# Kernel optimization log

Hardware: AMD Instinct MI355X
Metric: run time of the kernel (lower is better)

The kernel has to match this reference:

```python
import jax, jax.numpy as jnp
from jax import lax
import numpy as np

DIM = 256
QK = 256          # qk_dim defaults to dim
HEADS = 8
NWIN = 7
TOPK = 4
KS = 3            # side_dwconv


def setup_inputs() -> dict:
    key = jax.random.key(0)
    ks = jax.random.split(key, 8)
    B, H, W = 1, 112, 112
    s = lambda d: 1.0 / np.sqrt(d)
    return {
        "x": jax.random.normal(ks[0], (B, H, W, DIM), jnp.float32),
        # fused qkv linear: dim -> qk + qk + dim
        "w_qkv": jax.random.normal(ks[1], (DIM, 2 * QK + DIM), jnp.float32) * s(DIM),
        "b_qkv": jnp.zeros((2 * QK + DIM,), jnp.float32),
        # output projection
        "w_o": jax.random.normal(ks[2], (DIM, DIM), jnp.float32) * s(DIM),
        "b_o": jnp.zeros((DIM,), jnp.float32),
        # depthwise 3x3 lepe conv (HWIO with I=1, groups=dim)
        "lepe_w": jax.random.normal(ks[3], (KS, KS, 1, DIM), jnp.float32) * s(KS * KS),
        "lepe_b": jnp.zeros((DIM,), jnp.float32),
    }


def _win2img(t, B, H, W, c):
    # (B, p2, h, w, c) windows -> (B, H, W, c) image
    hw, ww = H // NWIN, W // NWIN
    t = t.reshape(B, NWIN, NWIN, hw, ww, c)
    return t.transpose(0, 1, 3, 2, 4, 5).reshape(B, H, W, c)


def reference(x, w_qkv, b_qkv, w_o, b_o, lepe_w, lepe_b):
    B, H, W, C = x.shape
    hw, ww = H // NWIN, W // NWIN
    p2, w2 = NWIN * NWIN, hw * ww
    hd_q, hd_v = QK // HEADS, DIM // HEADS
    scale = QK ** (-0.5)

    # partition into windows: (B, p2, hw, ww, C)
    xp = x.reshape(B, NWIN, hw, NWIN, ww, C).transpose(0, 1, 3, 2, 4, 5)
    xp = xp.reshape(B, p2, hw, ww, C)

    qkv = xp @ w_qkv + b_qkv
    q, kv = qkv[..., :QK], qkv[..., QK:]          # (B,p2,hw,ww,QK), (...,QK+DIM)

    q_pix = q.reshape(B, p2, w2, QK)
    kv_pix = kv.reshape(B, p2, w2, QK + DIM)      # identity kv_down

    # region-level routing (detached in original since diff_routing=False)
    q_win = lax.stop_gradient(q.mean((2, 3)))     # (B,p2,QK)
    k_win = lax.stop_gradient(kv[..., :QK].mean((2, 3)))
    logit = (q_win * scale) @ jnp.swapaxes(k_win, -1, -2)   # (B,p2,p2)
    top_logit, top_idx = lax.top_k(logit, TOPK)             # (B,p2,TOPK)
    r_weight = jax.nn.softmax(top_logit, axis=-1)           # unused: mul_weight='none'

    # gather top-k regions' KV: (B, p2, TOPK, w2, QK+DIM)
    kv_sel = jax.vmap(lambda kvb, idxb: kvb[idxb])(kv_pix, top_idx)

    k_sel = kv_sel[..., :QK].reshape(B, p2, TOPK * w2, HEADS, hd_q)
    v_sel = kv_sel[..., QK:].reshape(B, p2, TOPK * w2, HEADS, hd_v)
    qh = q_pix.reshape(B, p2, w2, HEADS, hd_q)

    attn = jnp.einsum('bpqhc,bpkhc->bphqk', qh * scale, k_sel)
    attn = jax.nn.softmax(attn, axis=-1)
    out = jnp.einsum('bphqk,bpkhc->bpqhc', attn, v_sel).reshape(B, p2, hw, ww, DIM)
    out = _win2img(out, B, H, W, DIM)

    # lepe: depthwise conv over v in image layout
    v_img = _win2img(kv[..., QK:], B, H, W, DIM)
    lepe = lax.conv_general_dilated(
        v_img, lepe_w, (1, 1), 'SAME',
        dimension_numbers=('NHWC', 'HWIO', 'NHWC'),
        feature_group_count=DIM) + lepe_b

    return (out + lepe) @ w_o + b_o
```

## Files before the change

### kernel.cpp

```cpp
#include <hip/hip_runtime.h>
#include <math.h>


typedef __bf16 bf16x8 __attribute__((ext_vector_type(8)));
typedef __bf16 bf16x4 __attribute__((ext_vector_type(4)));
typedef float f32x4 __attribute__((ext_vector_type(4)));

__global__ __launch_bounds__(64)
void pack1(const float* __restrict__ w_qkv, const float* __restrict__ w_o,
           __bf16* __restrict__ wtq, __bf16* __restrict__ wto,
           float* __restrict__ qkwin) {
    const int b = blockIdx.x;
    const int t = threadIdx.x;
    if (b < 768) {
        int n = b;
        int k = t * 4;
        bf16x4 o;
        o[0] = (__bf16)w_qkv[(k + 0) * 768 + n];
        o[1] = (__bf16)w_qkv[(k + 1) * 768 + n];
        o[2] = (__bf16)w_qkv[(k + 2) * 768 + n];
        o[3] = (__bf16)w_qkv[(k + 3) * 768 + n];
        *(bf16x4*)(wtq + (size_t)n * 256 + k) = o;
    } else if (b < 1024) {
        int n = b - 768;
        int k = t * 4;
        bf16x4 o;
        o[0] = (__bf16)w_o[(k + 0) * 256 + n];
        o[1] = (__bf16)w_o[(k + 1) * 256 + n];
        o[2] = (__bf16)w_o[(k + 2) * 256 + n];
        o[3] = (__bf16)w_o[(k + 3) * 256 + n];
        *(bf16x4*)(wto + (size_t)n * 256 + k) = o;
    } else {
        int idx = (b - 1024) * 64 + t;
        *(float4*)(qkwin + (size_t)idx * 4) = (float4){0.f, 0.f, 0.f, 0.f};
    }
}

template<int QKV>
__global__ __launch_bounds__(256)
void gemm_bf16(const __bf16* __restrict__ A,
               const float* __restrict__ Ax,
               const __bf16* __restrict__ Wt,
               const float* __restrict__ bias,
               float* __restrict__ C, int N,
               __bf16* __restrict__ Qp,
               __bf16* __restrict__ Kp,
               __bf16* __restrict__ vbf,
               __bf16* __restrict__ Vt,
               float* __restrict__ q_win,
               float* __restrict__ k_win) {
    const int t = threadIdx.x & 63;
    const int wv = threadIdx.x >> 6;
    const int l16 = t & 15, quad = t >> 4;
    const int m0 = blockIdx.x * 64;
    const int n0 = blockIdx.y * 128 + wv * 32;

    __shared__ __align__(16) char smem[33792];
    __bf16 (*const As)[264] = (__bf16(*)[264])smem;
    __bf16 (*const Vs)[72]  = (__bf16(*)[72])smem;

    if (QKV == 1) {
        const int p = m0 >> 8, pixbase = m0 & 255;
        const int rowbase0 = (p / 7) * 16 * 112 + (p % 7) * 16;
#pragma unroll
        for (int it = 0; it < 16; it++) {
            const int j = it * 1024 + threadIdx.x * 4;
            const int r = j >> 8, col = j & 255;
            const int pix = pixbase + r;
            const int ir = rowbase0 + (pix >> 4) * 112 + (pix & 15);
            const float4 f = *(const float4*)(Ax + (size_t)ir * 256 + col);
            bf16x4 o;
            o[0] = (__bf16)f.x; o[1] = (__bf16)f.y;
            o[2] = (__bf16)f.z; o[3] = (__bf16)f.w;
            *(bf16x4*)&As[r][col] = o;
        }
    } else {
#pragma unroll
        for (int it = 0; it < 8; it++) {
            const int j = it * 2048 + threadIdx.x * 8;
            const int r = j >> 8, col = j & 255;
            *(bf16x8*)&As[r][col] = *(const bf16x8*)(A + (size_t)(m0 + r) * 256 + col);
        }
    }
    __syncthreads();

    f32x4 acc[2][4];
#pragma unroll
    for (int km = 0; km < 2; km++)
#pragma unroll
        for (int nt = 0; nt < 4; nt++) acc[km][nt] = (f32x4){0.f, 0.f, 0.f, 0.f};

    bf16x8 Afc[2];
#pragma unroll
    for (int km = 0; km < 2; km++)
        Afc[km] = *(const bf16x8*)(Wt + (size_t)(n0 + km * 16 + l16) * 256 + quad * 8);

#pragma unroll
    for (int ks = 0; ks < 8; ks++) {
        bf16x8 Afn[2];
        const int ksn = (ks < 7) ? ks + 1 : 7;
#pragma unroll
        for (int km = 0; km < 2; km++)
            Afn[km] = *(const bf16x8*)(Wt + (size_t)(n0 + km * 16 + l16) * 256 + ksn * 32 + quad * 8);

        bf16x8 Bf[4];
#pragma unroll
        for (int nt = 0; nt < 4; nt++)
            Bf[nt] = *(const bf16x8*)&As[nt * 16 + l16][ks * 32 + quad * 8];

#pragma unroll
        for (int km = 0; km < 2; km++)
#pragma unroll
            for (int nt = 0; nt < 4; nt++)
                acc[km][nt] = __builtin_amdgcn_mfma_f32_16x16x32_bf16(
                    Afc[km], Bf[nt], acc[km][nt], 0, 0, 0);

#pragma unroll
        for (int km = 0; km < 2; km++) Afc[km] = Afn[km];
    }

    if (QKV == 1 && blockIdx.y >= 4) __syncthreads();

    float ws[2][4];
#pragma unroll
    for (int km = 0; km < 2; km++)
#pragma unroll
        for (int j = 0; j < 4; j++) ws[km][j] = 0.f;

#pragma unroll
    for (int km = 0; km < 2; km++) {
        const int n = n0 + km * 16 + quad * 4;
        float4 b4 = *(const float4*)(bias + n);
#pragma unroll
        for (int nt = 0; nt < 4; nt++) {
            const int m = m0 + nt * 16 + l16;
            float v0 = acc[km][nt][0] + b4.x;
            float v1 = acc[km][nt][1] + b4.y;
            float v2 = acc[km][nt][2] + b4.z;
            float v3 = acc[km][nt][3] + b4.w;
            if (QKV == 0) {
                float4 o = {v0, v1, v2, v3};
                *(float4*)(C + (size_t)m * N + n) = o;
            } else {
                const int p = m >> 8, pix = m & 255;
                if (n0 < 512) {
                    ws[km][0] += v0; ws[km][1] += v1;
                    ws[km][2] += v2; ws[km][3] += v3;
                }
                if (n0 < 256) {
                    const float s = 1.4426950408889634f / 16.0f;
                    int h = n >> 5, cc = n & 31;
                    bf16x4 o;
                    o[0] = (__bf16)(v0 * s); o[1] = (__bf16)(v1 * s);
                    o[2] = (__bf16)(v2 * s); o[3] = (__bf16)(v3 * s);
                    *(bf16x4*)(Qp + ((size_t)((p * 8 + h) * 256 + pix)) * 32 + cc) = o;
                } else if (n0 < 512) {
                    int n2 = n - 256;
                    int h = n2 >> 5, cc = n2 & 31;
                    bf16x4 o;
                    o[0] = (__bf16)v0; o[1] = (__bf16)v1;
                    o[2] = (__bf16)v2; o[3] = (__bf16)v3;
                    *(bf16x4*)(Kp + ((size_t)((p * 8 + h) * 256 + pix)) * 32 + cc) = o;
                } else {
                    int n2 = n - 512;
                    int imgrow = ((p / 7) * 16 + (pix >> 4)) * 112 + (p % 7) * 16 + (pix & 15);
                    bf16x4 o;
                    o[0] = (__bf16)v0; o[1] = (__bf16)v1;
                    o[2] = (__bf16)v2; o[3] = (__bf16)v3;
                    *(bf16x4*)(vbf + (size_t)imgrow * 256 + n2) = o;
                    const int cbase = wv * 32 + km * 16 + quad * 4;
                    const int pb = nt * 16 + l16;
                    Vs[cbase + 0][pb] = o[0];
                    Vs[cbase + 1][pb] = o[1];
                    Vs[cbase + 2][pb] = o[2];
                    Vs[cbase + 3][pb] = o[3];
                }
            }
        }
    }

    if (QKV == 1 && n0 < 512) {
        const int pblk = m0 >> 8;
#pragma unroll
        for (int km = 0; km < 2; km++) {
#pragma unroll
            for (int j = 0; j < 4; j++) {
                float s = ws[km][j];
                s += __shfl_xor(s, 1);
                s += __shfl_xor(s, 2);
                s += __shfl_xor(s, 4);
                s += __shfl_xor(s, 8);
                ws[km][j] = s;
            }
            if (l16 == 0) {
                const int n = n0 + km * 16 + quad * 4;
                float* dst = (n < 256) ? (q_win + pblk * 256 + n)
                                       : (k_win + pblk * 256 + (n - 256));
                atomicAdd(dst + 0, ws[km][0]);
                atomicAdd(dst + 1, ws[km][1]);
                atomicAdd(dst + 2, ws[km][2]);
                atomicAdd(dst + 3, ws[km][3]);
            }
        }
    }

    if (QKV == 1 && blockIdx.y >= 4) {
        __syncthreads();
        const int p_ = m0 >> 8, qt_ = (m0 >> 6) & 3;
        const int vb = blockIdx.y * 128 - 512;
#pragma unroll
        for (int rep = 0; rep < 4; rep++) {
            int id = rep * 256 + threadIdx.x;
            int row = id >> 3, c8 = (id & 7) * 8;
            int hh = (vb + row) >> 5, c32 = (vb + row) & 31;
            bf16x8 val = *(const bf16x8*)&Vs[row][c8];
            *(bf16x8*)(Vt + ((size_t)((p_ * 8 + hh) * 32 + c32)) * 256 + qt_ * 64 + c8) = val;
        }
    }
}

__global__ __launch_bounds__(64)
void routing_topk(const float* __restrict__ q_win,
                  const float* __restrict__ k_win,
                  int* __restrict__ top_idx) {
    const int r = blockIdx.x;
    const int j = threadIdx.x;
    __shared__ float vals[64];

    float d = -1e30f;
    if (j < 49) {
        const float4* qp = (const float4*)(q_win + r * 256);
        const float4* kp = (const float4*)(k_win + j * 256);
        float s = 0.f;
#pragma unroll
        for (int c = 0; c < 64; c++) {
            float4 a = qp[c], b = kp[c];
            s += a.x * b.x + a.y * b.y + a.z * b.z + a.w * b.w;
        }
        d = s;
    }
    vals[j] = d;
    __syncthreads();
    if (j == 0) {
        float bv0 = -1e30f, bv1 = -1e30f, bv2 = -1e30f, bv3 = -1e30f;
        int bi0 = 0, bi1 = 0, bi2 = 0, bi3 = 0;
        for (int q = 0; q < 49; q++) {
            float v = vals[q];
            if (v > bv0) {
                bv3 = bv2; bi3 = bi2; bv2 = bv1; bi2 = bi1; bv1 = bv0; bi1 = bi0;
                bv0 = v; bi0 = q;
            } else if (v > bv1) {
                bv3 = bv2; bi3 = bi2; bv2 = bv1; bi2 = bi1; bv1 = v; bi1 = q;
            } else if (v > bv2) {
                bv3 = bv2; bi3 = bi2; bv2 = v; bi2 = q;
            } else if (v > bv3) {
                bv3 = v; bi3 = q;
            }
        }
        top_idx[r * 4 + 0] = bi0;
        top_idx[r * 4 + 1] = bi1;
        top_idx[r * 4 + 2] = bi2;
        top_idx[r * 4 + 3] = bi3;
    }
}

#define PLDS_PITCH 68
#define HALO_PITCH 36

__global__ __launch_bounds__(256)
void attn_mfma(const __bf16* __restrict__ Qp,
               const __bf16* __restrict__ Kp,
               const __bf16* __restrict__ Vt,
               const int* __restrict__ top_idx,
               const __bf16* __restrict__ vbf,
               const float* __restrict__ lw,
               const float* __restrict__ lb,
               __bf16* __restrict__ prebf) {
    const int bb = blockIdx.x;
    const int qt = bb / 392;
    const int ph = bb - qt * 392;
    const int p = ph >> 3;
    const int h = ph & 7;
    const int t = threadIdx.x & 63;
    const int wv = threadIdx.x >> 6;
    const int l16 = t & 15, quad = t >> 4;

    __shared__ union {
        unsigned short Plds[4][64 * PLDS_PITCH];
        struct {
            f32x4 O[4][2][4][64];
            float l[4][4][64];
        } red;
        __bf16 Hs[108 * HALO_PITCH];
    } U;

    unsigned short* const Pw = U.Plds[wv];

    bf16x8 Qf[4];
#pragma unroll
    for (int nt = 0; nt < 4; nt++)
        Qf[nt] = *(const bf16x8*)(Qp + ((size_t)((p * 8 + h) * 256 + qt * 64 + nt * 16 + l16)) * 32 + quad * 8);

    const int sel = top_idx[p * 4 + wv];
    const __bf16* const Kb = Kp + ((size_t)(sel * 8 + h)) * 8192;
    const __bf16* const Vb = Vt + ((size_t)(sel * 8 + h)) * 8192;

    float lstate[4] = {0.f, 0.f, 0.f, 0.f};
    f32x4 O[2][4];
#pragma unroll
    for (int mt = 0; mt < 2; mt++)
#pragma unroll
        for (int nt = 0; nt < 4; nt++) O[mt][nt] = (f32x4){0.f, 0.f, 0.f, 0.f};

    bf16x8 Kf[4];
#pragma unroll
    for (int km = 0; km < 4; km++)
        Kf[km] = *(const bf16x8*)(Kb + (size_t)(km * 16 + l16) * 32 + quad * 8);

    for (int kc = 0; kc < 4; kc++) {
        const int kbase = kc * 64;

        bf16x8 Vf[2][2];
#pragma unroll
        for (int ks = 0; ks < 2; ks++)
#pragma unroll
            for (int mt = 0; mt < 2; mt++)
                Vf[ks][mt] = *(const bf16x8*)(Vb + (size_t)(mt * 16 + l16) * 256 + kbase + ks * 32 + quad * 8);

        const int kbn = (kc < 3 ? kc + 1 : 3) * 64;
        bf16x8 Kn[4];
#pragma unroll
        for (int km = 0; km < 4; km++)
            Kn[km] = *(const bf16x8*)(Kb + (size_t)(kbn + km * 16 + l16) * 32 + quad * 8);

#pragma unroll
        for (int nt = 0; nt < 4; nt++) {
            f32x4 S[4];
            __builtin_amdgcn_s_setprio(1);
#pragma unroll
            for (int km = 0; km < 4; km++)
                S[km] = __builtin_amdgcn_mfma_f32_16x16x32_bf16(
                    Kf[km], Qf[nt], (f32x4){0.f, 0.f, 0.f, 0.f}, 0, 0, 0);
            __builtin_amdgcn_s_setprio(0);

            float rs = 0.f;
#pragma unroll
            for (int km = 0; km < 4; km++) {
                union { unsigned short u[4]; ushort4 v; } pk;
#pragma unroll
                for (int r = 0; r < 4; r++) {
                    float pv = __builtin_amdgcn_exp2f(S[km][r]);
                    rs += pv;
                    pk.u[r] = __builtin_bit_cast(unsigned short, (__bf16)pv);
                }
                *(ushort4*)&Pw[(nt * 16 + l16) * PLDS_PITCH + km * 16 + quad * 4] = pk.v;
            }
            rs += __shfl_xor(rs, 16);
            rs += __shfl_xor(rs, 32);
            lstate[nt] += rs;
        }

#pragma unroll
        for (int ks = 0; ks < 2; ks++) {
#pragma unroll
            for (int nt = 0; nt < 4; nt++) {
                int idx = (nt * 16 + l16) * PLDS_PITCH + ks * 32 + quad * 8;
                union { ushort4 u4[2]; bf16x8 v; } pu;
                pu.u4[0] = *(const ushort4*)&Pw[idx];
                pu.u4[1] = *(const ushort4*)&Pw[idx + 4];
                __builtin_amdgcn_s_setprio(1);
#pragma unroll
                for (int mt = 0; mt < 2; mt++)
                    O[mt][nt] = __builtin_amdgcn_mfma_f32_16x16x32_bf16(
                        Vf[ks][mt], pu.v, O[mt][nt], 0, 0, 0);
                __builtin_amdgcn_s_setprio(0);
            }
        }

#pragma unroll
        for (int km = 0; km < 4; km++) Kf[km] = Kn[km];
    }

    __syncthreads();
#pragma unroll
    for (int mt = 0; mt < 2; mt++)
#pragma unroll
        for (int nt = 0; nt < 4; nt++)
            U.red.O[wv][mt][nt][t] = O[mt][nt];
#pragma unroll
    for (int nt = 0; nt < 4; nt++)
        U.red.l[wv][nt][t] = lstate[nt];
    __syncthreads();

    const int nt = wv;
    const float ltot = U.red.l[0][nt][t] + U.red.l[1][nt][t]
                     + U.red.l[2][nt][t] + U.red.l[3][nt][t];
    const float inv = 1.f / ltot;
    f32x4 Osum[2];
#pragma unroll
    for (int mt = 0; mt < 2; mt++) {
        f32x4 o = U.red.O[0][mt][nt][t];
#pragma unroll
        for (int v = 1; v < 4; v++) {
            f32x4 ov = U.red.O[v][mt][nt][t];
            o[0] += ov[0]; o[1] += ov[1]; o[2] += ov[2]; o[3] += ov[3];
        }
        Osum[mt] = o;
    }
    __syncthreads();

    const int pr = p / 7, pc = p % 7;
    if (threadIdx.x < 108) {
        const int i = threadIdx.x;
        int hy = i / 18, hx = i - hy * 18;
        int gy = pr * 16 + qt * 4 - 1 + hy;
        int gx = pc * 16 - 1 + hx;
        union { bf16x4 v4[8]; bf16x8 v8[4]; uint4 q[4]; } u;
        u.q[0] = (uint4){0u, 0u, 0u, 0u};
        u.q[1] = (uint4){0u, 0u, 0u, 0u};
        u.q[2] = (uint4){0u, 0u, 0u, 0u};
        u.q[3] = (uint4){0u, 0u, 0u, 0u};
        if (gy >= 0 && gy < 112 && gx >= 0 && gx < 112) {
            const __bf16* src = vbf + ((size_t)(gy * 112 + gx)) * 256 + h * 32;
            u.v8[0] = *(const bf16x8*)src;
            u.v8[1] = *(const bf16x8*)(src + 8);
            u.v8[2] = *(const bf16x8*)(src + 16);
            u.v8[3] = *(const bf16x8*)(src + 24);
        }
#pragma unroll
        for (int j = 0; j < 8; j++)
            *(bf16x4*)&U.Hs[i * HALO_PITCH + j * 4] = u.v4[j];
    }
    __syncthreads();

    const int himg = pr * 16 + qt * 4 + nt, wimg = pc * 16 + l16;
#pragma unroll
    for (int mt = 0; mt < 2; mt++) {
        const int c = h * 32 + mt * 16 + quad * 4;
        const float4 lbv = *(const float4*)(lb + c);
        float a0 = lbv.x, a1 = lbv.y, a2 = lbv.z, a3 = lbv.w;
#pragma unroll
        for (int dh = 0; dh < 3; dh++)
#pragma unroll
            for (int dw = 0; dw < 3; dw++) {
                const float4 w4 = *(const float4*)(lw + (dh * 3 + dw) * 256 + c);
                const bf16x4 v4 = *(const bf16x4*)&U.Hs[((nt + dh) * 18 + l16 + dw) * HALO_PITCH + mt * 16 + quad * 4];
                a0 += (float)v4[0] * w4.x;
                a1 += (float)v4[1] * w4.y;
                a2 += (float)v4[2] * w4.z;
                a3 += (float)v4[3] * w4.w;
            }
        bf16x4 ob;
        ob[0] = (__bf16)(Osum[mt][0] * inv + a0);
        ob[1] = (__bf16)(Osum[mt][1] * inv + a1);
        ob[2] = (__bf16)(Osum[mt][2] * inv + a2);
        ob[3] = (__bf16)(Osum[mt][3] * inv + a3);
        *(bf16x4*)(prebf + ((size_t)(himg * 112 + wimg)) * 256 + c) = ob;
    }
}

extern "C" void kernel_launch(void* const* d_in, const int* in_sizes, int n_in,
                              void* d_out, int out_size, void* d_ws, size_t ws_size,
                              hipStream_t stream) {
    const float* x      = (const float*)d_in[0];
    const float* w_qkv  = (const float*)d_in[1];
    const float* b_qkv  = (const float*)d_in[2];
    const float* w_o    = (const float*)d_in[3];
    const float* b_o    = (const float*)d_in[4];
    const float* lepe_w = (const float*)d_in[5];
    const float* lepe_b = (const float*)d_in[6];
    float* out = (float*)d_out;

    char* w = (char*)d_ws;
    __bf16* Qp    = (__bf16*)w; w += 6422528;
    __bf16* Kp    = (__bf16*)w; w += 6422528;
    __bf16* vbf   = (__bf16*)w; w += 6422528;
    __bf16* Vt    = (__bf16*)w; w += 6422528;
    __bf16* prebf = (__bf16*)w; w += 6422528;
    __bf16* wtq   = (__bf16*)w; w += 393216;
    __bf16* wto   = (__bf16*)w; w += 131072;
    float* q_win   = (float*)w; w += 12544 * 4;
    float* k_win   = (float*)w; w += 12544 * 4;
    int*   top_idx = (int*)w;

    pack1<<<768 + 256 + 98, 64, 0, stream>>>(w_qkv, w_o, wtq, wto, q_win);
    gemm_bf16<1><<<dim3(196, 6), 256, 0, stream>>>(nullptr, x, wtq, b_qkv,
                                                   nullptr, 0, Qp, Kp, vbf, Vt,
                                                   q_win, k_win);
    routing_topk<<<49, 64, 0, stream>>>(q_win, k_win, top_idx);
    attn_mfma<<<392 * 4, 256, 0, stream>>>(Qp, Kp, Vt, top_idx,
                                           vbf, lepe_w, lepe_b, prebf);
    gemm_bf16<0><<<dim3(196, 2), 256, 0, stream>>>(prebf, nullptr, wto, b_o,
                                                   out, 256, nullptr, nullptr, nullptr, nullptr,
                                                   nullptr, nullptr);
}
```

Measured before the change: 160.0 us.

## Software-pipeline QK softmax and PV MFMAs with double-buffered P tiles

Restructures the attention inner loop into a fully unrolled 16-step pipeline in which the QK^T plus exp stage for the next 16-query tile runs before the PV MFMAs of the current tile. The per-wave P buffer in LDS shrinks to two 16-row ping-pong slices. V fragments are now prefetched after the last PV of each chunk instead of at the start of the chunk. The goal is to interleave exp/LDS work with MFMA work and cut dependency stalls, at the cost of more live registers and a longer unrolled body.

```diff
diff --git a/kernel.cpp b/kernel.cpp
--- a/kernel.cpp
+++ b/kernel.cpp
@@ -286,7 +286,7 @@
     const int l16 = t & 15, quad = t >> 4;
 
     __shared__ union {
-        unsigned short Plds[4][64 * PLDS_PITCH];
+        unsigned short Plds[4][2][16 * PLDS_PITCH];
         struct {
             f32x4 O[4][2][4][64];
             float l[4][4][64];
@@ -294,8 +294,6 @@
         __bf16 Hs[108 * HALO_PITCH];
     } U;
 
-    unsigned short* const Pw = U.Plds[wv];
-
     bf16x8 Qf[4];
 #pragma unroll
     for (int nt = 0; nt < 4; nt++)
@@ -312,73 +310,90 @@
 #pragma unroll
         for (int nt = 0; nt < 4; nt++) O[mt][nt] = (f32x4){0.f, 0.f, 0.f, 0.f};
 
-    bf16x8 Kf[4];
+    bf16x8 Kf[4], Kn[4], Vf[2][2];
 #pragma unroll
     for (int km = 0; km < 4; km++)
         Kf[km] = *(const bf16x8*)(Kb + (size_t)(km * 16 + l16) * 32 + quad * 8);
-
-    for (int kc = 0; kc < 4; kc++) {
-        const int kbase = kc * 64;
-
-        bf16x8 Vf[2][2];
-#pragma unroll
-        for (int ks = 0; ks < 2; ks++)
+#pragma unroll
+    for (int ks = 0; ks < 2; ks++)
+#pragma unroll
+        for (int mt = 0; mt < 2; mt++)
+            Vf[ks][mt] = *(const bf16x8*)(Vb + (size_t)(mt * 16 + l16) * 256 + ks * 32 + quad * 8);
+
+    auto QKSM = [&](int ntv, int par) {
+        f32x4 S[4];
+        __builtin_amdgcn_s_setprio(1);
+#pragma unroll
+        for (int km = 0; km < 4; km++)
+            S[km] = __builtin_amdgcn_mfma_f32_16x16x32_bf16(
+                Kf[km], Qf[ntv], (f32x4){0.f, 0.f, 0.f, 0.f}, 0, 0, 0);
+        __builtin_amdgcn_s_setprio(0);
+        unsigned short* const Pp = U.Plds[wv][par];
+        float rs = 0.f;
+#pragma unroll
+        for (int km = 0; km < 4; km++) {
+            union { unsigned short u_[4]; ushort4 v; } pk;
+#pragma unroll
+            for (int r = 0; r < 4; r++) {
+                float pv = __builtin_amdgcn_exp2f(S[km][r]);
+                rs += pv;
+                pk.u_[r] = __builtin_bit_cast(unsigned short, (__bf16)pv);
+            }
+            *(ushort4*)&Pp[l16 * PLDS_PITCH + km * 16 + quad * 4] = pk.v;
+        }
+        rs += __shfl_xor(rs, 16);
+        rs += __shfl_xor(rs, 32);
+        lstate[ntv] += rs;
+    };
+
+    auto PV = [&](int ntv, int par) {
+        unsigned short* const Pp = U.Plds[wv][par];
+#pragma unroll
+        for (int ks = 0; ks < 2; ks++) {
+            const int idx = l16 * PLDS_PITCH + ks * 32 + quad * 8;
+            union { ushort4 u4[2]; bf16x8 v; } pu;
+            pu.u4[0] = *(const ushort4*)&Pp[idx];
+            pu.u4[1] = *(const ushort4*)&Pp[idx + 4];
+            __builtin_amdgcn_s_setprio(1);
 #pragma unroll
             for (int mt = 0; mt < 2; mt++)
-                Vf[ks][mt] = *(const bf16x8*)(Vb + (size_t)(mt * 16 + l16) * 256 + kbase + ks * 32 + quad * 8);
-
-        const int kbn = (kc < 3 ? kc + 1 : 3) * 64;
-        bf16x8 Kn[4];
-#pragma unroll
-        for (int km = 0; km < 4; km++)
-            Kn[km] = *(const bf16x8*)(Kb + (size_t)(kbn + km * 16 + l16) * 32 + quad * 8);
-
-#pragma unroll
-        for (int nt = 0; nt < 4; nt++) {
-            f32x4 S[4];
-            __builtin_amdgcn_s_setprio(1);
+                O[mt][ntv] = __builtin_amdgcn_mfma_f32_16x16x32_bf16(
+                    Vf[ks][mt], pu.v, O[mt][ntv], 0, 0, 0);
+            __builtin_amdgcn_s_setprio(0);
+        }
+    };
+
+    QKSM(0, 0);
+
+#pragma unroll
+    for (int u = 0; u < 16; u++) {
+        const int kc = u >> 2, nt = u & 3;
+        const int par = u & 1;
+
+        if (nt == 0 && kc < 3) {
 #pragma unroll
             for (int km = 0; km < 4; km++)
-                S[km] = __builtin_amdgcn_mfma_f32_16x16x32_bf16(
-                    Kf[km], Qf[nt], (f32x4){0.f, 0.f, 0.f, 0.f}, 0, 0, 0);
-            __builtin_amdgcn_s_setprio(0);
-
-            float rs = 0.f;
-#pragma unroll
-            for (int km = 0; km < 4; km++) {
-                union { unsigned short u[4]; ushort4 v; } pk;
-#pragma unroll
-                for (int r = 0; r < 4; r++) {
-                    float pv = __builtin_amdgcn_exp2f(S[km][r]);
-                    rs += pv;
-                    pk.u[r] = __builtin_bit_cast(unsigned short, (__bf16)pv);
-                }
-                *(ushort4*)&Pw[(nt * 16 + l16) * PLDS_PITCH + km * 16 + quad * 4] = pk.v;
-            }
-            rs += __shfl_xor(rs, 16);
-            rs += __shfl_xor(rs, 32);
-            lstate[nt] += rs;
-        }
-
-#pragma unroll
-        for (int ks = 0; ks < 2; ks++) {
-#pragma unroll
-            for (int nt = 0; nt < 4; nt++) {
-                int idx = (nt * 16 + l16) * PLDS_PITCH + ks * 32 + quad * 8;
-                union { ushort4 u4[2]; bf16x8 v; } pu;
-                pu.u4[0] = *(const ushort4*)&Pw[idx];
-                pu.u4[1] = *(const ushort4*)&Pw[idx + 4];
-                __builtin_amdgcn_s_setprio(1);
+                Kn[km] = *(const bf16x8*)(Kb + (size_t)((kc + 1) * 64 + km * 16 + l16) * 32 + quad * 8);
+        }
+
+        if (u < 15) {
+            const int ntn = (u + 1) & 3;
+            if (ntn == 0) {
+#pragma unroll
+                for (int km = 0; km < 4; km++) Kf[km] = Kn[km];
+            }
+            QKSM(ntn, par ^ 1);
+        }
+
+        PV(nt, par);
+
+        if (nt == 3 && kc < 3) {
+#pragma unroll
+            for (int ks = 0; ks < 2; ks++)
 #pragma unroll
                 for (int mt = 0; mt < 2; mt++)
-                    O[mt][nt] = __builtin_amdgcn_mfma_f32_16x16x32_bf16(
-                        Vf[ks][mt], pu.v, O[mt][nt], 0, 0, 0);
-                __builtin_amdgcn_s_setprio(0);
-            }
-        }
-
-#pragma unroll
-        for (int km = 0; km < 4; km++) Kf[km] = Kn[km];
+                    Vf[ks][mt] = *(const bf16x8*)(Vb + (size_t)(mt * 16 + l16) * 256 + (kc + 1) * 64 + ks * 32 + quad * 8);
+        }
     }
 
     __syncthreads();
```

Result: no change. 157.5 us (-1.5%).
